# Kernel tuning notes

Hardware: AMD Instinct MI355X
Metric: run time of the kernel (lower is better)

## Reference

```python
import jax, jax.numpy as jnp
import numpy as np

B = 64
H = W = 16
DIMS = [2048, 1024, 512, 256, 128, 1]


def setup_inputs() -> dict:
    key = jax.random.key(0)
    ks = jax.random.split(key, 11)
    inp = {"x": jax.random.normal(ks[0], (B, DIMS[0], H, W), dtype=jnp.float32)}
    for i in range(5):
        fan_in = DIMS[i]
        out = DIMS[i + 1]
        # per-sample weights [B, out, in, 1, 1], scaled ~1/sqrt(fan_in) to keep sigmoids unsaturated
        inp[f"fc{i+1}w"] = jax.random.normal(ks[1 + 2 * i], (B, out, fan_in, 1, 1), dtype=jnp.float32) / jnp.sqrt(jnp.float32(fan_in))
        inp[f"fc{i+1}b"] = jax.random.normal(ks[2 + 2 * i], (B, out), dtype=jnp.float32) * 0.1
    return inp


def _target_fc(h, w, b):
    # grouped 1x1 conv with groups=B == per-sample linear over channel dim
    # h: [B, in, H, W], w: [B, out, in, 1, 1], b: [B, out] -> [B, out, H, W]
    return jnp.einsum("boi,bihw->bohw", w[..., 0, 0], h) + b[:, :, None, None]


def reference(x, fc1w, fc1b, fc2w, fc2b, fc3w, fc3b, fc4w, fc4b, fc5w, fc5b):
    q = jax.nn.sigmoid(_target_fc(x, fc1w, fc1b))
    q = jax.nn.sigmoid(_target_fc(q, fc2w, fc2b))
    q = jax.nn.sigmoid(_target_fc(q, fc3w, fc3b))
    q = jax.nn.sigmoid(_target_fc(q, fc4w, fc4b))
    q = _target_fc(q, fc5w, fc5b)  # [B, 1, H, W]
    q = jnp.squeeze(q, axis=1)      # .squeeze() -> [B, H, W]
    return jax.nn.sigmoid(q)
```

## Files before the change

kernel.cpp:

```cpp
#include <hip/hip_runtime.h>
#include <hip/hip_bf16.h>
#include <hip/hip_fp16.h>


typedef __attribute__((ext_vector_type(4)))  float    f32x4;
typedef __attribute__((ext_vector_type(16))) float    f32x16;
typedef __attribute__((ext_vector_type(8)))  short    short8;
typedef __attribute__((ext_vector_type(4)))  short    short4v;
typedef __attribute__((ext_vector_type(8)))  _Float16 half8;

__device__ __forceinline__ unsigned short f2h_bits(float f) {
  return __builtin_bit_cast(unsigned short, (_Float16)f);
}
__device__ __forceinline__ float h2f(short h) {
  return (float)__builtin_bit_cast(_Float16, (unsigned short)h);
}

__global__ __launch_bounds__(256) void transpose_cvt(const float* __restrict__ X,
                                                     short* __restrict__ XT) {
  __shared__ float tile[32][33];
  const int b  = blockIdx.z;
  const int c0 = blockIdx.x * 32, s0 = blockIdx.y * 32;
  const int tl = threadIdx.x & 31, tw = threadIdx.x >> 5;
  const float* xp = X + ((size_t)b * 2048 + c0) * 256 + s0;
#pragma unroll
  for (int i = 0; i < 4; ++i) {
    const int c = tw * 4 + i;
    tile[c][tl] = xp[(size_t)c * 256 + tl];
  }
  __syncthreads();
  short* op = XT + ((size_t)(b * 256 + s0)) * 2048 + c0;
#pragma unroll
  for (int i = 0; i < 4; ++i) {
    const int s = tw * 4 + i;
    op[(size_t)s * 2048 + tl] = (short)f2h_bits(tile[tl][s]);
  }
}

struct WFrag { f32x4 v[8]; };

template <int M, int K, int WAVES, int NSPLIT>
__global__ __launch_bounds__(WAVES * 64, 2) void gemm_layer(
    const float* __restrict__ W, const float* __restrict__ bias,
    const short* __restrict__ Xin, short* __restrict__ Out) {
  constexpr int BK    = 64;
  constexpr int KH    = BK / 16;
  constexpr int NT    = K / BK;
  constexpr int NCG   = 8 / NSPLIT;
  constexpr int TILES = NCG * KH;
  constexpr int BM    = WAVES * 32;
  constexpr int MT    = M / BM;
  constexpr int TPW   = TILES / WAVES;
  constexpr int NS    = 256 / NSPLIT;
  constexpr int EPIW  = 40;

  __shared__ __align__(16) short lds[2][TILES * 512];
  __shared__ __align__(16) short epi[WAVES][32][EPIW];

  const int tid = threadIdx.x;
  const int w = tid >> 6, l = tid & 63;
  const int lr = l & 31;
  const int lh = l >> 5;

  const int per_b = MT * NSPLIT;
  const int b   = blockIdx.x / per_b;
  const int rem = blockIdx.x % per_b;
  const int mt  = rem / NSPLIT;
  const int ns  = rem % NSPLIT;
  const int m0  = mt * BM + w * 32;

  const float* Wb = W + ((size_t)b * M + m0) * K;
  const short* Xb = Xin + (size_t)b * 256 * K + (size_t)ns * NS * K;

  f32x16 acc[NCG] = {};

  auto stage = [&](int buf, int t) {
    const int k0 = t * BK;
#pragma unroll
    for (int i = 0; i < TPW; ++i) {
      const int T  = w * TPW + i;
      const int s  = (T / KH) * 32 + lr;
      const int kk = (T % KH) * 16 + (lh << 3);
      const short* src = Xb + (size_t)s * K + k0 + kk;
      __builtin_amdgcn_global_load_lds(
          (const __attribute__((address_space(1))) void*)src,
          (__attribute__((address_space(3))) void*)&lds[buf][T * 512],
          16, 0, 0);
    }
  };

  const float* wrow = Wb + (size_t)lr * K + (lh << 3);
  auto load_wfrag = [&](int t) {
    WFrag f;
#pragma unroll
    for (int h = 0; h < KH; ++h) {
      const float* wp = wrow + t * BK + h * 16;
      f.v[2 * h]     = *(const f32x4*)wp;
      f.v[2 * h + 1] = *(const f32x4*)(wp + 4);
    }
    return f;
  };

  WFrag wn;
  half8 wcH[KH];
  auto cvtW = [&]() {
#pragma unroll
    for (int h = 0; h < KH; ++h) {
#pragma unroll
      for (int j = 0; j < 4; ++j) {
        wcH[h][j]     = (_Float16)wn.v[2 * h][j];
        wcH[h][j + 4] = (_Float16)wn.v[2 * h + 1][j];
      }
    }
  };

  stage(0, 0);
  asm volatile("" ::: "memory");
  wn = load_wfrag(0);
  asm volatile("" ::: "memory");
  stage(1, 1);
  asm volatile("" ::: "memory");
  cvtW();
  wn = load_wfrag(1);
  asm volatile("" ::: "memory");
  asm volatile("s_barrier" ::: "memory");
  __builtin_amdgcn_sched_barrier(0);

  for (int t = 0; t < NT; ++t) {
    const int cur = t & 1;
#pragma unroll
    for (int h = 0; h < KH; ++h) {
#pragma unroll
      for (int cg = 0; cg < NCG; ++cg) {
        const short8 braw = *(const short8*)&lds[cur][(cg * KH + h) * 512 + l * 8];
        acc[cg] = __builtin_amdgcn_mfma_f32_32x32x16_f16(wcH[h], __builtin_bit_cast(half8, braw),
                                                         acc[cg], 0, 0, 0);
      }
    }
    if (t + 1 < NT) {
      asm volatile("s_waitcnt vmcnt(8)" ::: "memory");
      __builtin_amdgcn_sched_barrier(0);
      asm volatile("s_barrier" ::: "memory");
      __builtin_amdgcn_sched_barrier(0);
      if (t + 2 < NT) {
        stage(cur, t + 2);
        asm volatile("" ::: "memory");
      }
      cvtW();
      if (t + 2 < NT) {
        wn = load_wfrag(t + 2);
        asm volatile("" ::: "memory");
      }
    }
  }

  float brow[16];
#pragma unroll
  for (int r = 0; r < 16; ++r) {
    const int row = (r & 3) + 8 * (r >> 2) + (lh << 2);
    brow[r] = bias[(size_t)b * M + m0 + row];
  }
  const int s_loc = l >> 1, hi = l & 1;
#pragma unroll
  for (int cg = 0; cg < NCG; ++cg) {
#pragma unroll
    for (int rg = 0; rg < 4; ++rg) {
      short4v pk;
#pragma unroll
      for (int j = 0; j < 4; ++j) {
        const int r = rg * 4 + j;
        float v = acc[cg][r] + brow[r];
        v = 1.0f / (1.0f + __expf(-v));
        pk[j] = (short)f2h_bits(v);
      }
      *(short4v*)&epi[w][lr][rg * 8 + (lh << 2)] = pk;
    }
    const short8 r0 = *(const short8*)&epi[w][s_loc][hi * 16];
    const short8 r1 = *(const short8*)&epi[w][s_loc][hi * 16 + 8];
    short* op = Out + ((size_t)b * 256 + ns * NS + cg * 32 + s_loc) * M + m0 + hi * 16;
    *(short8*)op       = r0;
    *(short8*)(op + 8) = r1;
  }
}

__global__ __launch_bounds__(256) void fc5_sig(const float* __restrict__ W5,
                                               const float* __restrict__ B5,
                                               const short* __restrict__ H4,
                                               float* __restrict__ out) {
  const int tid = blockIdx.x * 256 + threadIdx.x;
  const int oi = tid >> 3;
  const int r  = tid & 7;
  const int b  = oi >> 8;
  const short* hp = H4 + ((size_t)oi << 7) + r * 16;
  const float* wp = W5 + b * 128 + r * 16;
  const short8 hh0 = *(const short8*)hp;
  const short8 hh1 = *(const short8*)(hp + 8);
  const f32x4 w0 = *(const f32x4*)wp;
  const f32x4 w1 = *(const f32x4*)(wp + 4);
  const f32x4 w2 = *(const f32x4*)(wp + 8);
  const f32x4 w3 = *(const f32x4*)(wp + 12);
  float a = 0.f;
#pragma unroll
  for (int j = 0; j < 4; ++j) a += h2f(hh0[j]) * w0[j];
#pragma unroll
  for (int j = 0; j < 4; ++j) a += h2f(hh0[j + 4]) * w1[j];
#pragma unroll
  for (int j = 0; j < 4; ++j) a += h2f(hh1[j]) * w2[j];
#pragma unroll
  for (int j = 0; j < 4; ++j) a += h2f(hh1[j + 4]) * w3[j];
  a += __shfl_xor(a, 1);
  a += __shfl_xor(a, 2);
  a += __shfl_xor(a, 4);
  if (r == 0) out[oi] = 1.0f / (1.0f + __expf(-(a + B5[b])));
}

extern "C" void kernel_launch(void* const* d_in, const int* in_sizes, int n_in,
                              void* d_out, int out_size, void* d_ws, size_t ws_size,
                              hipStream_t stream) {
  const float* x  = (const float*)d_in[0];
  const float* w1 = (const float*)d_in[1];  const float* b1 = (const float*)d_in[2];
  const float* w2 = (const float*)d_in[3];  const float* b2 = (const float*)d_in[4];
  const float* w3 = (const float*)d_in[5];  const float* b3 = (const float*)d_in[6];
  const float* w4 = (const float*)d_in[7];  const float* b4 = (const float*)d_in[8];
  const float* w5 = (const float*)d_in[9];  const float* b5 = (const float*)d_in[10];

  char* ws = (char*)d_ws;
  short* bufA = (short*)ws;
  short* bufB = (short*)(ws + (size_t)67108864);
  float* out  = (float*)d_out;

  transpose_cvt<<<dim3(64, 8, 64), 256, 0, stream>>>(x, bufA);
  gemm_layer<1024, 2048, 4, 1><<<512, 256, 0, stream>>>(w1, b1, bufA, bufB);
  gemm_layer<512, 1024, 2, 1><<<512, 128, 0, stream>>>(w2, b2, bufB, bufA);
  gemm_layer<256, 512, 2, 2><<<512, 128, 0, stream>>>(w3, b3, bufA, bufB);
  gemm_layer<128, 256, 1, 2><<<512, 64, 0, stream>>>(w4, b4, bufB, bufA);
  fc5_sig<<<512, 256, 0, stream>>>(w5, b5, bufA, out);
}
```

Before: 340.9 us.

## Fuse final fc5 layer into layer-4 GEMM epilogue and rebalance wave splits

Removes the separate fc5_sig kernel. Layer 4 now runs with four waves covering all 128 output rows and an eight-way column split, so each block holds full hidden vectors in its LDS epilogue buffer and computes the final dot product and sigmoid in place. This avoids writing layer-4 activations to global memory and skips one launch. Layers 2 and 3 also move to four waves with larger column splits, which changes per-block work, staging tile count and occupancy.

```diff
diff --git a/kernel.cpp b/kernel.cpp
--- a/kernel.cpp
+++ b/kernel.cpp
@@ -39,10 +39,12 @@
 
 struct WFrag { f32x4 v[8]; };
 
-template <int M, int K, int WAVES, int NSPLIT>
+template <int M, int K, int WAVES, int NSPLIT, bool FUSE5>
 __global__ __launch_bounds__(WAVES * 64, 2) void gemm_layer(
     const float* __restrict__ W, const float* __restrict__ bias,
-    const short* __restrict__ Xin, short* __restrict__ Out) {
+    const short* __restrict__ Xin, short* __restrict__ Out,
+    const float* __restrict__ W5, const float* __restrict__ B5,
+    float* __restrict__ out5) {
   constexpr int BK    = 64;
   constexpr int KH    = BK / 16;
   constexpr int NT    = K / BK;
@@ -175,43 +177,39 @@
       }
       *(short4v*)&epi[w][lr][rg * 8 + (lh << 2)] = pk;
     }
-    const short8 r0 = *(const short8*)&epi[w][s_loc][hi * 16];
-    const short8 r1 = *(const short8*)&epi[w][s_loc][hi * 16 + 8];
-    short* op = Out + ((size_t)b * 256 + ns * NS + cg * 32 + s_loc) * M + m0 + hi * 16;
-    *(short8*)op       = r0;
-    *(short8*)(op + 8) = r1;
-  }
-}
-
-__global__ __launch_bounds__(256) void fc5_sig(const float* __restrict__ W5,
-                                               const float* __restrict__ B5,
-                                               const short* __restrict__ H4,
-                                               float* __restrict__ out) {
-  const int tid = blockIdx.x * 256 + threadIdx.x;
-  const int oi = tid >> 3;
-  const int r  = tid & 7;
-  const int b  = oi >> 8;
-  const short* hp = H4 + ((size_t)oi << 7) + r * 16;
-  const float* wp = W5 + b * 128 + r * 16;
-  const short8 hh0 = *(const short8*)hp;
-  const short8 hh1 = *(const short8*)(hp + 8);
-  const f32x4 w0 = *(const f32x4*)wp;
-  const f32x4 w1 = *(const f32x4*)(wp + 4);
-  const f32x4 w2 = *(const f32x4*)(wp + 8);
-  const f32x4 w3 = *(const f32x4*)(wp + 12);
-  float a = 0.f;
-#pragma unroll
-  for (int j = 0; j < 4; ++j) a += h2f(hh0[j]) * w0[j];
-#pragma unroll
-  for (int j = 0; j < 4; ++j) a += h2f(hh0[j + 4]) * w1[j];
-#pragma unroll
-  for (int j = 0; j < 4; ++j) a += h2f(hh1[j]) * w2[j];
-#pragma unroll
-  for (int j = 0; j < 4; ++j) a += h2f(hh1[j + 4]) * w3[j];
-  a += __shfl_xor(a, 1);
-  a += __shfl_xor(a, 2);
-  a += __shfl_xor(a, 4);
-  if (r == 0) out[oi] = 1.0f / (1.0f + __expf(-(a + B5[b])));
+    if (!FUSE5) {
+      const short8 r0 = *(const short8*)&epi[w][s_loc][hi * 16];
+      const short8 r1 = *(const short8*)&epi[w][s_loc][hi * 16 + 8];
+      short* op = Out + ((size_t)b * 256 + ns * NS + cg * 32 + s_loc) * M + m0 + hi * 16;
+      *(short8*)op       = r0;
+      *(short8*)(op + 8) = r1;
+    }
+  }
+
+  if (FUSE5) {
+    __syncthreads();
+    const int s_ = tid >> 3, r_ = tid & 7;
+    const short8 h0 = *(const short8*)&epi[r_ >> 1][s_][(r_ & 1) * 16];
+    const short8 h1 = *(const short8*)&epi[r_ >> 1][s_][(r_ & 1) * 16 + 8];
+    const float* wp = W5 + b * 128 + r_ * 16;
+    const f32x4 w0 = *(const f32x4*)wp;
+    const f32x4 w1 = *(const f32x4*)(wp + 4);
+    const f32x4 w2 = *(const f32x4*)(wp + 8);
+    const f32x4 w3 = *(const f32x4*)(wp + 12);
+    float a = 0.f;
+#pragma unroll
+    for (int j = 0; j < 4; ++j) a += h2f(h0[j]) * w0[j];
+#pragma unroll
+    for (int j = 0; j < 4; ++j) a += h2f(h0[j + 4]) * w1[j];
+#pragma unroll
+    for (int j = 0; j < 4; ++j) a += h2f(h1[j]) * w2[j];
+#pragma unroll
+    for (int j = 0; j < 4; ++j) a += h2f(h1[j + 4]) * w3[j];
+    a += __shfl_xor(a, 1);
+    a += __shfl_xor(a, 2);
+    a += __shfl_xor(a, 4);
+    if (r_ == 0) out5[b * 256 + ns * NS + s_] = 1.0f / (1.0f + __expf(-(a + B5[b])));
+  }
 }
 
 extern "C" void kernel_launch(void* const* d_in, const int* in_sizes, int n_in,
@@ -230,9 +228,12 @@
   float* out  = (float*)d_out;
 
   transpose_cvt<<<dim3(64, 8, 64), 256, 0, stream>>>(x, bufA);
-  gemm_layer<1024, 2048, 4, 1><<<512, 256, 0, stream>>>(w1, b1, bufA, bufB);
-  gemm_layer<512, 1024, 2, 1><<<512, 128, 0, stream>>>(w2, b2, bufB, bufA);
-  gemm_layer<256, 512, 2, 2><<<512, 128, 0, stream>>>(w3, b3, bufA, bufB);
-  gemm_layer<128, 256, 1, 2><<<512, 64, 0, stream>>>(w4, b4, bufB, bufA);
-  fc5_sig<<<512, 256, 0, stream>>>(w5, b5, bufA, out);
-}
+  gemm_layer<1024, 2048, 4, 1, false><<<512, 256, 0, stream>>>(
+      w1, b1, bufA, bufB, nullptr, nullptr, nullptr);
+  gemm_layer<512, 1024, 4, 2, false><<<512, 256, 0, stream>>>(
+      w2, b2, bufB, bufA, nullptr, nullptr, nullptr);
+  gemm_layer<256, 512, 4, 4, false><<<512, 256, 0, stream>>>(
+      w3, b3, bufA, bufB, nullptr, nullptr, nullptr);
+  gemm_layer<128, 256, 4, 8, true><<<512, 256, 0, stream>>>(
+      w4, b4, bufB, nullptr, w5, b5, out);
+}
```

Measured after the change: 345.2 us. Within noise of the previous version (+1.3%).
